# Optimization experiments

Hardware: AMD Instinct MI355X
Metric: run time of the kernel (lower is better)

## Reference

```python
import jax, jax.numpy as jnp
import numpy as np

B, S, E, H = 4, 2048, 1024, 16
D = E // H  # head dim = 64


def setup_inputs() -> dict:
    key = jax.random.key(0)
    ks = jax.random.split(key, 9)
    s_in = 1.0 / np.sqrt(E)
    return {
        "x": jax.random.normal(ks[0], (B, S, E), dtype=jnp.float32),
        # stacked per-head projection weights, acting as x @ W + b
        "Wq": jax.random.normal(ks[1], (H, E, D), dtype=jnp.float32) * s_in,
        "bq": jax.random.normal(ks[2], (H, D), dtype=jnp.float32) * 0.01,
        "Wk": jax.random.normal(ks[3], (H, E, D), dtype=jnp.float32) * s_in,
        "bk": jax.random.normal(ks[4], (H, D), dtype=jnp.float32) * 0.01,
        "Wv": jax.random.normal(ks[5], (H, E, D), dtype=jnp.float32) * s_in,
        "bv": jax.random.normal(ks[6], (H, D), dtype=jnp.float32) * 0.01,
        "Wo": jax.random.normal(ks[7], (E, E), dtype=jnp.float32) * s_in,
        "bo": jax.random.normal(ks[8], (E,), dtype=jnp.float32) * 0.01,
    }


def reference(x, Wq, bq, Wk, bk, Wv, bv, Wo, bo):
    # Batched per-head projections (equivalent to the per-head nn.Linear loop)
    q = jnp.einsum("bse,hed->bhsd", x, Wq) + bq[None, :, None, :]
    k = jnp.einsum("bse,hed->bhsd", x, Wk) + bk[None, :, None, :]
    v = jnp.einsum("bse,hed->bhsd", x, Wv) + bv[None, :, None, :]
    scale = 1.0 / jnp.sqrt(jnp.asarray(D, dtype=x.dtype))
    scores = jnp.einsum("bhsd,bhtd->bhst", q, k) * scale  # [B,H,S,S]
    attn = jax.nn.softmax(scores, axis=-1)
    ctx = jnp.einsum("bhst,bhtd->bhsd", attn, v)  # [B,H,S,D]
    # torch.cat over heads along last dim -> [B,S,H*D]=[B,S,E]
    ctx = jnp.transpose(ctx, (0, 2, 1, 3)).reshape(x.shape[0], x.shape[1], E)
    return ctx @ Wo + bo
```

## Files before the change

### kernel.cpp

```cpp
#include <hip/hip_runtime.h>
#include <math.h>

#define B_ 4
#define S_ 2048
#define E_ 1024
#define H_ 16
#define D_ 64
#define BH_ (B_ * H_)

#define SCALE_LOG2E 0.18033688011112042f

typedef short short8 __attribute__((ext_vector_type(8)));
typedef float f32x4 __attribute__((ext_vector_type(4)));
typedef float f32x16 __attribute__((ext_vector_type(16)));

static __device__ __forceinline__ unsigned short f2bf(float f) {
    unsigned int u = __float_as_uint(f);
    unsigned int r = (u + 0x7fffu + ((u >> 16) & 1u)) >> 16;
    return (unsigned short)r;
}

static __device__ __forceinline__ unsigned int pack_bf16_trunc(float hi, float lo) {
    return __builtin_amdgcn_perm(__float_as_uint(hi), __float_as_uint(lo), 0x07060302u);
}

static __device__ __forceinline__ void gl_lds16(const unsigned short* g, unsigned short* l) {
    __builtin_amdgcn_global_load_lds(
        (const __attribute__((address_space(1))) unsigned int*)g,
        (__attribute__((address_space(3))) unsigned int*)l, 16, 0, 0);
}


__global__ __launch_bounds__(256) void xcvt_kernel(
    const float* __restrict__ x, unsigned short* __restrict__ Xb)
{
    size_t i = ((size_t)blockIdx.x * 256 + threadIdx.x) * 8;
    float4 a = *(const float4*)&x[i];
    float4 b = *(const float4*)&x[i + 4];
    ushort4 u0, u1;
    u0.x = f2bf(a.x); u0.y = f2bf(a.y); u0.z = f2bf(a.z); u0.w = f2bf(a.w);
    u1.x = f2bf(b.x); u1.y = f2bf(b.y); u1.z = f2bf(b.z); u1.w = f2bf(b.w);
    *(ushort4*)&Xb[i]     = u0;
    *(ushort4*)&Xb[i + 4] = u1;
}

__global__ __launch_bounds__(256) void wtrans_qkv_kernel(
    const float* __restrict__ Wq, const float* __restrict__ Wk,
    const float* __restrict__ Wv, unsigned short* __restrict__ Wt)
{
    __shared__ float t[32][33];
    const int tx = threadIdx.x & 31, ty = threadIdx.x >> 5;
    const int r0 = blockIdx.x * 32, c0 = blockIdx.y * 32;
    const int z = blockIdx.z, mtx = z >> 4, h = z & 15;
    const float* s = (mtx == 0 ? Wq : (mtx == 1 ? Wk : Wv)) + (size_t)h * E_ * D_;
    const float scale = (mtx == 0) ? SCALE_LOG2E : 1.0f;
    unsigned short* d = Wt + (size_t)mtx * E_ * E_ + (size_t)h * D_ * E_;
#pragma unroll
    for (int i = 0; i < 4; ++i)
        t[ty + i * 8][tx] = s[(size_t)(r0 + ty + i * 8) * D_ + c0 + tx];
    __syncthreads();
#pragma unroll
    for (int i = 0; i < 4; ++i)
        d[(size_t)(c0 + ty + i * 8) * E_ + r0 + tx] = f2bf(t[tx][ty + i * 8] * scale);
}

__global__ __launch_bounds__(256) void wtrans_kernel(
    const float* __restrict__ src, unsigned short* __restrict__ dst, int R, int C)
{
    __shared__ float t[32][33];
    const int tx = threadIdx.x & 31, ty = threadIdx.x >> 5;
    const int r0 = blockIdx.x * 32, c0 = blockIdx.y * 32;
#pragma unroll
    for (int i = 0; i < 4; ++i)
        t[ty + i * 8][tx] = src[(size_t)(r0 + ty + i * 8) * C + c0 + tx];
    __syncthreads();
#pragma unroll
    for (int i = 0; i < 4; ++i)
        dst[(size_t)(c0 + ty + i * 8) * R + r0 + tx] = f2bf(t[tx][ty + i * 8]);
}

__global__ __launch_bounds__(256) void qkv_gemm_kernel(
    const unsigned short* __restrict__ Xb, const unsigned short* __restrict__ Wt,
    const float* __restrict__ bq, const float* __restrict__ bk,
    const float* __restrict__ bv,
    unsigned short* __restrict__ Qh, unsigned short* __restrict__ Kh,
    unsigned short* __restrict__ Vth)
{
    __shared__ unsigned short As[2][128 * 64];
    __shared__ unsigned short Bs[2][128 * 64];
    const int tid = threadIdx.x;
    const int lane = tid & 63, wid = tid >> 6;
    const int quad = lane >> 4, lc = lane & 15;
    const int wm = wid >> 1, wn = wid & 1;
    const int m0 = blockIdx.y * 128, n0 = blockIdx.x * 128;
    const int l8 = lane >> 3;
    const int sch = ((lane & 7) ^ l8) * 8;

    f32x4 acc[4][4];
#pragma unroll
    for (int mt = 0; mt < 4; ++mt)
#pragma unroll
        for (int nt = 0; nt < 4; ++nt)
            acc[mt][nt] = (f32x4){0.f, 0.f, 0.f, 0.f};

#pragma unroll
    for (int i = 0; i < 4; ++i) {
        int rw = wid * 32 + i * 8;
        gl_lds16(&Xb[(size_t)(m0 + rw + l8) * E_ + sch], &As[0][rw * 64]);
        gl_lds16(&Wt[(size_t)(n0 + rw + l8) * E_ + sch], &Bs[0][rw * 64]);
    }
    __syncthreads();

    for (int k0 = 0; k0 < E_; k0 += 64) {
        const int cur = (k0 >> 6) & 1;
        if (k0 + 64 < E_) {
#pragma unroll
            for (int i = 0; i < 4; ++i) {
                int rw = wid * 32 + i * 8;
                gl_lds16(&Xb[(size_t)(m0 + rw + l8) * E_ + k0 + 64 + sch], &As[cur ^ 1][rw * 64]);
                gl_lds16(&Wt[(size_t)(n0 + rw + l8) * E_ + k0 + 64 + sch], &Bs[cur ^ 1][rw * 64]);
            }
        }
#pragma unroll
        for (int kc = 0; kc < 2; ++kc) {
            short8 a[4], bfr[4];
#pragma unroll
            for (int mt = 0; mt < 4; ++mt)
                a[mt] = *(const short8*)&As[cur][(wm * 64 + mt * 16 + lc) * 64 +
                                                (((kc * 4 + quad) ^ (lc & 7)) << 3)];
#pragma unroll
            for (int nt = 0; nt < 4; ++nt)
                bfr[nt] = *(const short8*)&Bs[cur][(wn * 64 + nt * 16 + lc) * 64 +
                                                  (((kc * 4 + quad) ^ (lc & 7)) << 3)];
#pragma unroll
            for (int mt = 0; mt < 4; ++mt)
#pragma unroll
                for (int nt = 0; nt < 4; ++nt)
                    acc[mt][nt] = __builtin_amdgcn_mfma_f32_16x16x32_bf16(
                        a[mt], bfr[nt], acc[mt][nt], 0, 0, 0);
        }
        __syncthreads();
    }

    const int nb = n0 + wn * 64;
    const int mtx = nb >> 10;
    const int h = (nb >> 6) & 15;
    const int sg0 = m0 + wm * 64;
    const int bb_ = sg0 >> 11;
    const int bhv = bb_ * H_ + h;
    if (mtx < 2) {
        const float bsc = (mtx == 0) ? SCALE_LOG2E : 1.0f;
        const float* bias = (mtx == 0 ? bq : bk) + h * D_;
        unsigned short* Out = (mtx == 0) ? Qh : Kh;
        const size_t obase = (size_t)bhv * (S_ / 32) * 2048;
#pragma unroll
        for (int nt = 0; nt < 4; ++nt) {
            int d = nt * 16 + lc;
            int hi_ = (lc >> 3) & 1, j = lc & 7;
            float bb = bias[d] * bsc;
#pragma unroll
            for (int mt = 0; mt < 4; ++mt)
#pragma unroll
                for (int r = 0; r < 4; ++r) {
                    int ss = (sg0 + mt * 16 + quad * 4 + r) & (S_ - 1);
                    Out[obase + ((size_t)(ss >> 5) * 4 + nt) * 512 +
                        ((ss & 31) * 2 + hi_) * 8 + j] = f2bf(acc[mt][nt][r] + bb);
                }
        }
    } else {
        const float* bias = bv + h * D_;
        const size_t obase = (size_t)bhv * (S_ / 64) * 4096;
        const int t64 = (sg0 & (S_ - 1)) >> 6;
        const int hi_ = quad >> 1, j0 = (quad & 1) * 4;
#pragma unroll
        for (int nt = 0; nt < 4; ++nt) {
            int d = nt * 16 + lc;
            int dsub = d >> 5, l31d = d & 31;
            float bb = bias[d];
#pragma unroll
            for (int mt = 0; mt < 4; ++mt) {
                ushort4 u;
                u.x = f2bf(acc[mt][nt][0] + bb);
                u.y = f2bf(acc[mt][nt][1] + bb);
                u.z = f2bf(acc[mt][nt][2] + bb);
                u.w = f2bf(acc[mt][nt][3] + bb);
                *(ushort4*)&Vth[obase + ((size_t)t64 * 8 + mt * 2 + dsub) * 512 +
                                (l31d * 2 + hi_) * 8 + j0] = u;
            }
        }
    }
}

__global__ __launch_bounds__(256, 4) void attn_kernel(
    const unsigned short* __restrict__ Qh, const unsigned short* __restrict__ Kh,
    const unsigned short* __restrict__ Vth, unsigned short* __restrict__ Ch)
{
    __shared__ unsigned short ks[2][8 * 512];
    __shared__ unsigned short vt[2][8 * 512];
    const int tid = threadIdx.x;
    const int lane = tid & 63, wid = tid >> 6;
    const int l31 = lane & 31, hi = lane >> 5;
    const int bh = blockIdx.x, b = bh >> 4, h = bh & 15;
    const int q0 = blockIdx.y * 128;
    const size_t qkbase = (size_t)bh * (S_ / 32) * 2048;
    const size_t vbase  = (size_t)bh * (S_ / 64) * 4096;
    const int rdoff = (l31 * 2 + hi) * 8;
    const int ldoff = lane * 8;

    unsigned short* qstage = &ks[0][0];
    {
        const int t32 = (q0 >> 5) + wid;
#pragma unroll
        for (int kc = 0; kc < 4; ++kc)
            gl_lds16(&Qh[qkbase + ((size_t)t32 * 4 + kc) * 512 + ldoff],
                     &qstage[(wid * 4 + kc) * 512]);
    }
    __syncthreads();
    short8 qf[4];
#pragma unroll
    for (int kc = 0; kc < 4; ++kc)
        qf[kc] = *(const short8*)&qstage[(wid * 4 + kc) * 512 + rdoff];
    __syncthreads();

#pragma unroll
    for (int i = 0; i < 2; ++i) {
        int sk = wid * 2 + i;
        int kb = sk >> 2, kc = sk & 3;
        gl_lds16(&Kh[qkbase + ((size_t)kb * 4 + kc) * 512 + ldoff], &ks[0][sk * 512]);
        gl_lds16(&Vth[vbase + (size_t)sk * 512 + ldoff], &vt[0][sk * 512]);
    }
    __syncthreads();

    short8 ones;
#pragma unroll
    for (int i = 0; i < 8; ++i) ones[i] = (short)0x3F80;

    f32x16 ctx[2], lacc;
#pragma unroll
    for (int i = 0; i < 16; ++i) { ctx[0][i] = 0.f; ctx[1][i] = 0.f; lacc[i] = 0.f; }

    for (int kt = 0; kt < S_; kt += 64) {
        const int cur = (kt >> 6) & 1;
        if (kt + 64 < S_) {
            const int ktn = kt + 64;
#pragma unroll
            for (int i = 0; i < 2; ++i) {
                int sk = wid * 2 + i;
                int kb = sk >> 2, kc = sk & 3;
                gl_lds16(&Kh[qkbase + ((size_t)((ktn >> 5) + kb) * 4 + kc) * 512 + ldoff],
                         &ks[cur ^ 1][sk * 512]);
                gl_lds16(&Vth[vbase + ((size_t)(ktn >> 6) * 8 + sk) * 512 + ldoff],
                         &vt[cur ^ 1][sk * 512]);
            }
        }

#pragma unroll
        for (int kb = 0; kb < 2; ++kb) {
            f32x16 st;
#pragma unroll
            for (int i = 0; i < 16; ++i) st[i] = 0.f;
            __builtin_amdgcn_s_setprio(1);
#pragma unroll
            for (int kc = 0; kc < 4; ++kc) {
                short8 kf = *(const short8*)&ks[cur][(kb * 4 + kc) * 512 + rdoff];
                st = __builtin_amdgcn_mfma_f32_32x32x16_bf16(kf, qf[kc], st, 0, 0, 0);
            }
            __builtin_amdgcn_s_setprio(0);

#pragma unroll
            for (int ks16 = 0; ks16 < 2; ++ks16) {
                float e0 = __builtin_amdgcn_exp2f(st[8 * ks16 + 0]);
                float e1 = __builtin_amdgcn_exp2f(st[8 * ks16 + 1]);
                float e2 = __builtin_amdgcn_exp2f(st[8 * ks16 + 2]);
                float e3 = __builtin_amdgcn_exp2f(st[8 * ks16 + 3]);
                float e4 = __builtin_amdgcn_exp2f(st[8 * ks16 + 4]);
                float e5 = __builtin_amdgcn_exp2f(st[8 * ks16 + 5]);
                float e6 = __builtin_amdgcn_exp2f(st[8 * ks16 + 6]);
                float e7 = __builtin_amdgcn_exp2f(st[8 * ks16 + 7]);
                unsigned int w0 = pack_bf16_trunc(e1, e0);
                unsigned int w1 = pack_bf16_trunc(e3, e2);
                unsigned int w2 = pack_bf16_trunc(e5, e4);
                unsigned int w3 = pack_bf16_trunc(e7, e6);
                asm("v_permlane32_swap_b32 %0, %1" : "+v"(w0), "+v"(w2));
                asm("v_permlane32_swap_b32 %0, %1" : "+v"(w1), "+v"(w3));
                union { unsigned int u[4]; short8 s; } pu;
                pu.u[0] = w0; pu.u[1] = w1; pu.u[2] = w2; pu.u[3] = w3;
                const short8 pf = pu.s;

                __builtin_amdgcn_s_setprio(1);
                lacc = __builtin_amdgcn_mfma_f32_32x32x16_bf16(pf, ones, lacc, 0, 0, 0);
#pragma unroll
                for (int dsub = 0; dsub < 2; ++dsub) {
                    short8 vf = *(const short8*)&vt[cur][((kb * 2 + ks16) * 2 + dsub) * 512 + rdoff];
                    ctx[dsub] = __builtin_amdgcn_mfma_f32_32x32x16_bf16(
                        pf, vf, ctx[dsub], 0, 0, 0);
                }
                __builtin_amdgcn_s_setprio(0);
            }
        }
        __syncthreads();
    }

#pragma unroll
    for (int r = 0; r < 16; ++r) {
        float inv = 1.f / lacc[r];
        int q = q0 + wid * 32 + (r & 3) + ((r >> 2) << 3) + hi * 4;
        size_t rowbase = ((size_t)b * S_ + q) * E_ + h * D_;
        Ch[rowbase + l31]      = f2bf(ctx[0][r] * inv);
        Ch[rowbase + 32 + l31] = f2bf(ctx[1][r] * inv);
    }
}

__global__ __launch_bounds__(256) void out_proj_kernel(
    const unsigned short* __restrict__ Ch, const unsigned short* __restrict__ Wot,
    const float* __restrict__ bo, float* __restrict__ out)
{
    __shared__ unsigned short As[2][128 * 64];
    __shared__ unsigned short Bs[2][128 * 64];
    const int tid = threadIdx.x;
    const int lane = tid & 63, wid = tid >> 6;
    const int quad = lane >> 4, lc = lane & 15;
    const int wm = wid >> 1, wn = wid & 1;
    const int m0 = blockIdx.y * 128, n0 = blockIdx.x * 128;
    const int l8 = lane >> 3;
    const int sch = ((lane & 7) ^ l8) * 8;

    f32x4 acc[4][4];
#pragma unroll
    for (int mt = 0; mt < 4; ++mt)
#pragma unroll
        for (int nt = 0; nt < 4; ++nt)
            acc[mt][nt] = (f32x4){0.f, 0.f, 0.f, 0.f};

#pragma unroll
    for (int i = 0; i < 4; ++i) {
        int rw = wid * 32 + i * 8;
        gl_lds16(&Ch[(size_t)(m0 + rw + l8) * E_ + sch], &As[0][rw * 64]);
        gl_lds16(&Wot[(size_t)(n0 + rw + l8) * E_ + sch], &Bs[0][rw * 64]);
    }
    __syncthreads();

    for (int k0 = 0; k0 < E_; k0 += 64) {
        const int cur = (k0 >> 6) & 1;
        if (k0 + 64 < E_) {
#pragma unroll
            for (int i = 0; i < 4; ++i) {
                int rw = wid * 32 + i * 8;
                gl_lds16(&Ch[(size_t)(m0 + rw + l8) * E_ + k0 + 64 + sch], &As[cur ^ 1][rw * 64]);
                gl_lds16(&Wot[(size_t)(n0 + rw + l8) * E_ + k0 + 64 + sch], &Bs[cur ^ 1][rw * 64]);
            }
        }
#pragma unroll
        for (int kc = 0; kc < 2; ++kc) {
            short8 a[4], bfr[4];
#pragma unroll
            for (int mt = 0; mt < 4; ++mt)
                a[mt] = *(const short8*)&As[cur][(wm * 64 + mt * 16 + lc) * 64 +
                                                (((kc * 4 + quad) ^ (lc & 7)) << 3)];
#pragma unroll
            for (int nt = 0; nt < 4; ++nt)
                bfr[nt] = *(const short8*)&Bs[cur][(wn * 64 + nt * 16 + lc) * 64 +
                                                  (((kc * 4 + quad) ^ (lc & 7)) << 3)];
#pragma unroll
            for (int mt = 0; mt < 4; ++mt)
#pragma unroll
                for (int nt = 0; nt < 4; ++nt)
                    acc[mt][nt] = __builtin_amdgcn_mfma_f32_16x16x32_bf16(
                        a[mt], bfr[nt], acc[mt][nt], 0, 0, 0);
        }
        __syncthreads();
    }

#pragma unroll
    for (int mt = 0; mt < 4; ++mt)
#pragma unroll
        for (int nt = 0; nt < 4; ++nt) {
            int n = n0 + wn * 64 + nt * 16 + lc;
            float bb = bo[n];
#pragma unroll
            for (int r = 0; r < 4; ++r) {
                int row = m0 + wm * 64 + mt * 16 + quad * 4 + r;
                out[(size_t)row * E_ + n] = acc[mt][nt][r] + bb;
            }
        }
}

extern "C" void kernel_launch(void* const* d_in, const int* in_sizes, int n_in,
                              void* d_out, int out_size, void* d_ws, size_t ws_size,
                              hipStream_t stream)
{
    const float* x  = (const float*)d_in[0];
    const float* Wq = (const float*)d_in[1];
    const float* bq = (const float*)d_in[2];
    const float* Wk = (const float*)d_in[3];
    const float* bk = (const float*)d_in[4];
    const float* Wv = (const float*)d_in[5];
    const float* bv = (const float*)d_in[6];
    const float* Wo = (const float*)d_in[7];
    const float* bo = (const float*)d_in[8];
    (void)in_sizes; (void)n_in; (void)out_size; (void)ws_size;

    const size_t N = (size_t)BH_ * S_ * D_;
    unsigned short* Wt  = (unsigned short*)d_ws;
    unsigned short* Wot = Wt + (size_t)3072 * 1024;
    unsigned short* Xb  = Wot + (size_t)1024 * 1024;
    unsigned short* Qh  = Xb + N;
    unsigned short* Kh  = Qh + N;
    unsigned short* Vth = Kh + N;
    unsigned short* Ch  = Vth + N;

    xcvt_kernel<<<dim3(4096), 256, 0, stream>>>(x, Xb);
    wtrans_qkv_kernel<<<dim3(32, 2, 48), 256, 0, stream>>>(Wq, Wk, Wv, Wt);
    wtrans_kernel<<<dim3(32, 32, 1), 256, 0, stream>>>(Wo, Wot, E_, E_);

    qkv_gemm_kernel<<<dim3(24, 64), 256, 0, stream>>>(Xb, Wt, bq, bk, bv, Qh, Kh, Vth);
    attn_kernel<<<dim3(64, 16), 256, 0, stream>>>(Qh, Kh, Vth, Ch);
    out_proj_kernel<<<dim3(8, 64), 256, 0, stream>>>(Ch, Wot, bo, (float*)d_out);
}
```

Measured before the change: 279.5 us.

## Shrink attention blocks to two waves with 32-key tiles and direct Q loads

Each attention block now has 128 threads covering 64 queries instead of 256 threads covering 128, which doubles the grid. The key/value tile shrinks from 64 to 32 keys per iteration, so LDS use per block drops: one wave stages K and the other stages V. Q fragments are read straight from global memory into registers, removing the LDS staging pass and its two barriers. The aim is more resident blocks per CU and a shorter prologue, at the cost of twice as many K/V fetches from L2 overall and twice as many barriers per key processed.

```diff
diff --git a/kernel.cpp b/kernel.cpp
--- a/kernel.cpp
+++ b/kernel.cpp
@@ -191,45 +191,37 @@
     }
 }
 
-__global__ __launch_bounds__(256, 4) void attn_kernel(
+__global__ __launch_bounds__(128, 4) void attn_kernel(
     const unsigned short* __restrict__ Qh, const unsigned short* __restrict__ Kh,
     const unsigned short* __restrict__ Vth, unsigned short* __restrict__ Ch)
 {
-    __shared__ unsigned short ks[2][8 * 512];
-    __shared__ unsigned short vt[2][8 * 512];
+    __shared__ unsigned short ks[2][4 * 512];
+    __shared__ unsigned short vt[2][4 * 512];
     const int tid = threadIdx.x;
     const int lane = tid & 63, wid = tid >> 6;
     const int l31 = lane & 31, hi = lane >> 5;
     const int bh = blockIdx.x, b = bh >> 4, h = bh & 15;
-    const int q0 = blockIdx.y * 128;
-    const size_t qkbase = (size_t)bh * (S_ / 32) * 2048;
-    const size_t vbase  = (size_t)bh * (S_ / 64) * 4096;
+    const int q0 = blockIdx.y * 64;
+    const size_t gbase = (size_t)bh * (S_ / 32) * 2048;
     const int rdoff = (l31 * 2 + hi) * 8;
     const int ldoff = lane * 8;
 
-    unsigned short* qstage = &ks[0][0];
+    short8 qf[4];
     {
         const int t32 = (q0 >> 5) + wid;
 #pragma unroll
         for (int kc = 0; kc < 4; ++kc)
-            gl_lds16(&Qh[qkbase + ((size_t)t32 * 4 + kc) * 512 + ldoff],
-                     &qstage[(wid * 4 + kc) * 512]);
+            qf[kc] = *(const short8*)&Qh[gbase + ((size_t)t32 * 4 + kc) * 512 + rdoff];
+    }
+
+#pragma unroll
+    for (int i = 0; i < 4; ++i) {
+        if (wid == 0)
+            gl_lds16(&Kh[gbase + (size_t)i * 512 + ldoff], &ks[0][i * 512]);
+        else
+            gl_lds16(&Vth[gbase + (size_t)i * 512 + ldoff], &vt[0][i * 512]);
     }
     __syncthreads();
-    short8 qf[4];
-#pragma unroll
-    for (int kc = 0; kc < 4; ++kc)
-        qf[kc] = *(const short8*)&qstage[(wid * 4 + kc) * 512 + rdoff];
-    __syncthreads();
-
-#pragma unroll
-    for (int i = 0; i < 2; ++i) {
-        int sk = wid * 2 + i;
-        int kb = sk >> 2, kc = sk & 3;
-        gl_lds16(&Kh[qkbase + ((size_t)kb * 4 + kc) * 512 + ldoff], &ks[0][sk * 512]);
-        gl_lds16(&Vth[vbase + (size_t)sk * 512 + ldoff], &vt[0][sk * 512]);
-    }
-    __syncthreads();
 
     short8 ones;
 #pragma unroll
@@ -239,64 +231,59 @@
 #pragma unroll
     for (int i = 0; i < 16; ++i) { ctx[0][i] = 0.f; ctx[1][i] = 0.f; lacc[i] = 0.f; }
 
-    for (int kt = 0; kt < S_; kt += 64) {
-        const int cur = (kt >> 6) & 1;
-        if (kt + 64 < S_) {
-            const int ktn = kt + 64;
-#pragma unroll
-            for (int i = 0; i < 2; ++i) {
-                int sk = wid * 2 + i;
-                int kb = sk >> 2, kc = sk & 3;
-                gl_lds16(&Kh[qkbase + ((size_t)((ktn >> 5) + kb) * 4 + kc) * 512 + ldoff],
-                         &ks[cur ^ 1][sk * 512]);
-                gl_lds16(&Vth[vbase + ((size_t)(ktn >> 6) * 8 + sk) * 512 + ldoff],
-                         &vt[cur ^ 1][sk * 512]);
-            }
-        }
-
-#pragma unroll
-        for (int kb = 0; kb < 2; ++kb) {
-            f32x16 st;
-#pragma unroll
-            for (int i = 0; i < 16; ++i) st[i] = 0.f;
+    for (int kt = 0; kt < S_; kt += 32) {
+        const int cur = (kt >> 5) & 1;
+        if (kt + 32 < S_) {
+            const size_t tb = gbase + ((size_t)((kt >> 5) + 1) * 4) * 512;
+#pragma unroll
+            for (int i = 0; i < 4; ++i) {
+                if (wid == 0)
+                    gl_lds16(&Kh[tb + (size_t)i * 512 + ldoff], &ks[cur ^ 1][i * 512]);
+                else
+                    gl_lds16(&Vth[tb + (size_t)i * 512 + ldoff], &vt[cur ^ 1][i * 512]);
+            }
+        }
+
+        f32x16 st;
+#pragma unroll
+        for (int i = 0; i < 16; ++i) st[i] = 0.f;
+        __builtin_amdgcn_s_setprio(1);
+#pragma unroll
+        for (int kc = 0; kc < 4; ++kc) {
+            short8 kf = *(const short8*)&ks[cur][kc * 512 + rdoff];
+            st = __builtin_amdgcn_mfma_f32_32x32x16_bf16(kf, qf[kc], st, 0, 0, 0);
+        }
+        __builtin_amdgcn_s_setprio(0);
+
+#pragma unroll
+        for (int ks16 = 0; ks16 < 2; ++ks16) {
+            float e0 = __builtin_amdgcn_exp2f(st[8 * ks16 + 0]);
+            float e1 = __builtin_amdgcn_exp2f(st[8 * ks16 + 1]);
+            float e2 = __builtin_amdgcn_exp2f(st[8 * ks16 + 2]);
+            float e3 = __builtin_amdgcn_exp2f(st[8 * ks16 + 3]);
+            float e4 = __builtin_amdgcn_exp2f(st[8 * ks16 + 4]);
+            float e5 = __builtin_amdgcn_exp2f(st[8 * ks16 + 5]);
+            float e6 = __builtin_amdgcn_exp2f(st[8 * ks16 + 6]);
+            float e7 = __builtin_amdgcn_exp2f(st[8 * ks16 + 7]);
+            unsigned int w0 = pack_bf16_trunc(e1, e0);
+            unsigned int w1 = pack_bf16_trunc(e3, e2);
+            unsigned int w2 = pack_bf16_trunc(e5, e4);
+            unsigned int w3 = pack_bf16_trunc(e7, e6);
+            asm("v_permlane32_swap_b32 %0, %1" : "+v"(w0), "+v"(w2));
+            asm("v_permlane32_swap_b32 %0, %1" : "+v"(w1), "+v"(w3));
+            union { unsigned int u[4]; short8 s; } pu;
+            pu.u[0] = w0; pu.u[1] = w1; pu.u[2] = w2; pu.u[3] = w3;
+            const short8 pf = pu.s;
+
             __builtin_amdgcn_s_setprio(1);
-#pragma unroll
-            for (int kc = 0; kc < 4; ++kc) {
-                short8 kf = *(const short8*)&ks[cur][(kb * 4 + kc) * 512 + rdoff];
-                st = __builtin_amdgcn_mfma_f32_32x32x16_bf16(kf, qf[kc], st, 0, 0, 0);
+            lacc = __builtin_amdgcn_mfma_f32_32x32x16_bf16(pf, ones, lacc, 0, 0, 0);
+#pragma unroll
+            for (int dsub = 0; dsub < 2; ++dsub) {
+                short8 vf = *(const short8*)&vt[cur][(ks16 * 2 + dsub) * 512 + rdoff];
+                ctx[dsub] = __builtin_amdgcn_mfma_f32_32x32x16_bf16(
+                    pf, vf, ctx[dsub], 0, 0, 0);
             }
             __builtin_amdgcn_s_setprio(0);
-
-#pragma unroll
-            for (int ks16 = 0; ks16 < 2; ++ks16) {
-                float e0 = __builtin_amdgcn_exp2f(st[8 * ks16 + 0]);
-                float e1 = __builtin_amdgcn_exp2f(st[8 * ks16 + 1]);
-                float e2 = __builtin_amdgcn_exp2f(st[8 * ks16 + 2]);
-                float e3 = __builtin_amdgcn_exp2f(st[8 * ks16 + 3]);
-                float e4 = __builtin_amdgcn_exp2f(st[8 * ks16 + 4]);
-                float e5 = __builtin_amdgcn_exp2f(st[8 * ks16 + 5]);
-                float e6 = __builtin_amdgcn_exp2f(st[8 * ks16 + 6]);
-                float e7 = __builtin_amdgcn_exp2f(st[8 * ks16 + 7]);
-                unsigned int w0 = pack_bf16_trunc(e1, e0);
-                unsigned int w1 = pack_bf16_trunc(e3, e2);
-                unsigned int w2 = pack_bf16_trunc(e5, e4);
-                unsigned int w3 = pack_bf16_trunc(e7, e6);
-                asm("v_permlane32_swap_b32 %0, %1" : "+v"(w0), "+v"(w2));
-                asm("v_permlane32_swap_b32 %0, %1" : "+v"(w1), "+v"(w3));
-                union { unsigned int u[4]; short8 s; } pu;
-                pu.u[0] = w0; pu.u[1] = w1; pu.u[2] = w2; pu.u[3] = w3;
-                const short8 pf = pu.s;
-
-                __builtin_amdgcn_s_setprio(1);
-                lacc = __builtin_amdgcn_mfma_f32_32x32x16_bf16(pf, ones, lacc, 0, 0, 0);
-#pragma unroll
-                for (int dsub = 0; dsub < 2; ++dsub) {
-                    short8 vf = *(const short8*)&vt[cur][((kb * 2 + ks16) * 2 + dsub) * 512 + rdoff];
-                    ctx[dsub] = __builtin_amdgcn_mfma_f32_32x32x16_bf16(
-                        pf, vf, ctx[dsub], 0, 0, 0);
-                }
-                __builtin_amdgcn_s_setprio(0);
-            }
         }
         __syncthreads();
     }
@@ -414,6 +401,6 @@
     wtrans_kernel<<<dim3(32, 32, 1), 256, 0, stream>>>(Wo, Wot, E_, E_);
 
     qkv_gemm_kernel<<<dim3(24, 64), 256, 0, stream>>>(Xb, Wt, bq, bk, bv, Qh, Kh, Vth);
-    attn_kernel<<<dim3(64, 16), 256, 0, stream>>>(Qh, Kh, Vth, Ch);
+    attn_kernel<<<dim3(64, 32), 128, 0, stream>>>(Qh, Kh, Vth, Ch);
     out_proj_kernel<<<dim3(8, 64), 256, 0, stream>>>(Ch, Wot, bo, (float*)d_out);
 }
```

New measurement: 285.4 us. 1.02x slower.

## Replace row-sum MFMA with VALU accumulation and load Q fragments directly

Applied to the files above, without the earlier changes.

The softmax denominator is now accumulated with scalar adds of the exponentials per lane, replacing the extra MFMA against a ones vector. Each query row's total is combined across the two half-wavefronts with permlane32 swap and shared through LDS at the end. Q fragments are read straight from global memory into registers instead of staged through LDS with two barriers. The two score MFMA chains are issued back to back before the exp/PV work to give more independent MFMAs. This removes a third of the PV-stage MFMAs but adds VALU adds, and the sum now uses unrounded fp32 exps rather than the truncated bf16 values used in PV.

```diff
diff --git a/kernel.cpp b/kernel.cpp
--- a/kernel.cpp
+++ b/kernel.cpp
@@ -202,42 +202,30 @@
     const int l31 = lane & 31, hi = lane >> 5;
     const int bh = blockIdx.x, b = bh >> 4, h = bh & 15;
     const int q0 = blockIdx.y * 128;
-    const size_t qkbase = (size_t)bh * (S_ / 32) * 2048;
-    const size_t vbase  = (size_t)bh * (S_ / 64) * 4096;
+    const size_t gbase = (size_t)bh * (S_ / 32) * 2048;
     const int rdoff = (l31 * 2 + hi) * 8;
     const int ldoff = lane * 8;
 
-    unsigned short* qstage = &ks[0][0];
+    short8 qf[4];
     {
         const int t32 = (q0 >> 5) + wid;
 #pragma unroll
         for (int kc = 0; kc < 4; ++kc)
-            gl_lds16(&Qh[qkbase + ((size_t)t32 * 4 + kc) * 512 + ldoff],
-                     &qstage[(wid * 4 + kc) * 512]);
-    }
-    __syncthreads();
-    short8 qf[4];
-#pragma unroll
-    for (int kc = 0; kc < 4; ++kc)
-        qf[kc] = *(const short8*)&qstage[(wid * 4 + kc) * 512 + rdoff];
-    __syncthreads();
+            qf[kc] = *(const short8*)&Qh[gbase + ((size_t)t32 * 4 + kc) * 512 + rdoff];
+    }
 
 #pragma unroll
     for (int i = 0; i < 2; ++i) {
         int sk = wid * 2 + i;
-        int kb = sk >> 2, kc = sk & 3;
-        gl_lds16(&Kh[qkbase + ((size_t)kb * 4 + kc) * 512 + ldoff], &ks[0][sk * 512]);
-        gl_lds16(&Vth[vbase + (size_t)sk * 512 + ldoff], &vt[0][sk * 512]);
-    }
-    __syncthreads();
-
-    short8 ones;
-#pragma unroll
-    for (int i = 0; i < 8; ++i) ones[i] = (short)0x3F80;
-
-    f32x16 ctx[2], lacc;
-#pragma unroll
-    for (int i = 0; i < 16; ++i) { ctx[0][i] = 0.f; ctx[1][i] = 0.f; lacc[i] = 0.f; }
+        gl_lds16(&Kh[gbase + (size_t)sk * 512 + ldoff], &ks[0][sk * 512]);
+        gl_lds16(&Vth[gbase + (size_t)sk * 512 + ldoff], &vt[0][sk * 512]);
+    }
+    __syncthreads();
+
+    f32x16 ctx[2];
+    float lsum = 0.f;
+#pragma unroll
+    for (int i = 0; i < 16; ++i) { ctx[0][i] = 0.f; ctx[1][i] = 0.f; }
 
     for (int kt = 0; kt < S_; kt += 64) {
         const int cur = (kt >> 6) & 1;
@@ -246,37 +234,41 @@
 #pragma unroll
             for (int i = 0; i < 2; ++i) {
                 int sk = wid * 2 + i;
-                int kb = sk >> 2, kc = sk & 3;
-                gl_lds16(&Kh[qkbase + ((size_t)((ktn >> 5) + kb) * 4 + kc) * 512 + ldoff],
+                gl_lds16(&Kh[gbase + ((size_t)((ktn >> 5) + (sk >> 2)) * 4 + (sk & 3)) * 512 + ldoff],
                          &ks[cur ^ 1][sk * 512]);
-                gl_lds16(&Vth[vbase + ((size_t)(ktn >> 6) * 8 + sk) * 512 + ldoff],
+                gl_lds16(&Vth[gbase + ((size_t)(ktn >> 6) * 8 + sk) * 512 + ldoff],
                          &vt[cur ^ 1][sk * 512]);
             }
         }
 
-#pragma unroll
-        for (int kb = 0; kb < 2; ++kb) {
-            f32x16 st;
-#pragma unroll
-            for (int i = 0; i < 16; ++i) st[i] = 0.f;
-            __builtin_amdgcn_s_setprio(1);
-#pragma unroll
-            for (int kc = 0; kc < 4; ++kc) {
-                short8 kf = *(const short8*)&ks[cur][(kb * 4 + kc) * 512 + rdoff];
-                st = __builtin_amdgcn_mfma_f32_32x32x16_bf16(kf, qf[kc], st, 0, 0, 0);
-            }
-            __builtin_amdgcn_s_setprio(0);
-
+        f32x16 st0, st1;
+#pragma unroll
+        for (int i = 0; i < 16; ++i) { st0[i] = 0.f; st1[i] = 0.f; }
+        __builtin_amdgcn_s_setprio(1);
+#pragma unroll
+        for (int kc = 0; kc < 4; ++kc) {
+            short8 kf0 = *(const short8*)&ks[cur][(0 * 4 + kc) * 512 + rdoff];
+            st0 = __builtin_amdgcn_mfma_f32_32x32x16_bf16(kf0, qf[kc], st0, 0, 0, 0);
+        }
+#pragma unroll
+        for (int kc = 0; kc < 4; ++kc) {
+            short8 kf1 = *(const short8*)&ks[cur][(1 * 4 + kc) * 512 + rdoff];
+            st1 = __builtin_amdgcn_mfma_f32_32x32x16_bf16(kf1, qf[kc], st1, 0, 0, 0);
+        }
+        __builtin_amdgcn_s_setprio(0);
+
+        auto process = [&](const f32x16& ST, int KB) {
 #pragma unroll
             for (int ks16 = 0; ks16 < 2; ++ks16) {
-                float e0 = __builtin_amdgcn_exp2f(st[8 * ks16 + 0]);
-                float e1 = __builtin_amdgcn_exp2f(st[8 * ks16 + 1]);
-                float e2 = __builtin_amdgcn_exp2f(st[8 * ks16 + 2]);
-                float e3 = __builtin_amdgcn_exp2f(st[8 * ks16 + 3]);
-                float e4 = __builtin_amdgcn_exp2f(st[8 * ks16 + 4]);
-                float e5 = __builtin_amdgcn_exp2f(st[8 * ks16 + 5]);
-                float e6 = __builtin_amdgcn_exp2f(st[8 * ks16 + 6]);
-                float e7 = __builtin_amdgcn_exp2f(st[8 * ks16 + 7]);
+                float e0 = __builtin_amdgcn_exp2f(ST[8 * ks16 + 0]);
+                float e1 = __builtin_amdgcn_exp2f(ST[8 * ks16 + 1]);
+                float e2 = __builtin_amdgcn_exp2f(ST[8 * ks16 + 2]);
+                float e3 = __builtin_amdgcn_exp2f(ST[8 * ks16 + 3]);
+                float e4 = __builtin_amdgcn_exp2f(ST[8 * ks16 + 4]);
+                float e5 = __builtin_amdgcn_exp2f(ST[8 * ks16 + 5]);
+                float e6 = __builtin_amdgcn_exp2f(ST[8 * ks16 + 6]);
+                float e7 = __builtin_amdgcn_exp2f(ST[8 * ks16 + 7]);
+                lsum += ((e0 + e1) + (e2 + e3)) + ((e4 + e5) + (e6 + e7));
                 unsigned int w0 = pack_bf16_trunc(e1, e0);
                 unsigned int w1 = pack_bf16_trunc(e3, e2);
                 unsigned int w2 = pack_bf16_trunc(e5, e4);
@@ -288,23 +280,33 @@
                 const short8 pf = pu.s;
 
                 __builtin_amdgcn_s_setprio(1);
-                lacc = __builtin_amdgcn_mfma_f32_32x32x16_bf16(pf, ones, lacc, 0, 0, 0);
 #pragma unroll
                 for (int dsub = 0; dsub < 2; ++dsub) {
-                    short8 vf = *(const short8*)&vt[cur][((kb * 2 + ks16) * 2 + dsub) * 512 + rdoff];
+                    short8 vf = *(const short8*)&vt[cur][((KB * 2 + ks16) * 2 + dsub) * 512 + rdoff];
                     ctx[dsub] = __builtin_amdgcn_mfma_f32_32x32x16_bf16(
                         pf, vf, ctx[dsub], 0, 0, 0);
                 }
                 __builtin_amdgcn_s_setprio(0);
             }
-        }
+        };
+        process(st0, 0);
+        process(st1, 1);
         __syncthreads();
     }
 
+    float* lsh = (float*)&ks[0][0];
+    {
+        float a = lsum, bx = lsum;
+        asm("v_permlane32_swap_b32 %0, %1" : "+v"(a), "+v"(bx));
+        float ltot = lsum + (hi ? a : bx);
+        if (hi == 0) lsh[wid * 32 + l31] = ltot;
+    }
+    __syncthreads();
 #pragma unroll
     for (int r = 0; r < 16; ++r) {
-        float inv = 1.f / lacc[r];
-        int q = q0 + wid * 32 + (r & 3) + ((r >> 2) << 3) + hi * 4;
+        int qr = (r & 3) + ((r >> 2) << 3) + hi * 4;
+        float inv = 1.f / lsh[wid * 32 + qr];
+        int q = q0 + wid * 32 + qr;
         size_t rowbase = ((size_t)b * S_ + q) * E_ + h * D_;
         Ch[rowbase + l31]      = f2bf(ctx[0][r] * inv);
         Ch[rowbase + 32 + l31] = f2bf(ctx[1][r] * inv);
```

Measured after the change: 273.1 us. 1.02x faster.
